# Kernel optimization log

Measured on AMD Instinct MI355X. Metric: run time of the kernel, lower is better.

Reference implementation:

```python
import jax, jax.numpy as jnp
import numpy as np

B, W, LOCAL, GLOBAL = 32, 16, 64, 64
EMB, HIDDEN, OUT, NLAYERS = 256, 512, 64, 3
T = 128  # output_len


def setup_inputs() -> dict:
    key = jax.random.key(0)
    ks = jax.random.split(key, 16)
    s = 0.05
    inp = {
        "z_t": jax.random.normal(ks[0], (B, W, LOCAL), jnp.float32),
        "z_g": jax.random.normal(ks[1], (B, GLOBAL), jnp.float32),
        # embedding: Linear(local+global -> 256, bias=False), torch layout (out,in)
        "w_emb": jax.random.normal(ks[2], (EMB, LOCAL + GLOBAL), jnp.float32) * s,
        # GRU(input_size=1, hidden=256); input is all-zeros so w_ih contributes
        # nothing (only its bias b_ih matters) -> faithfully omit w_ih.
        "gru_w_hh": jax.random.normal(ks[3], (3 * EMB, EMB), jnp.float32) * s,
        "gru_b_ih": jax.random.normal(ks[4], (3 * EMB,), jnp.float32) * s,
        "gru_b_hh": jax.random.normal(ks[5], (3 * EMB,), jnp.float32) * s,
        "mlp_w1": jax.random.normal(ks[6], (HIDDEN, EMB), jnp.float32) * s,
        "mlp_b1": jax.random.normal(ks[7], (HIDDEN,), jnp.float32) * s,
        "mlp_w2": jax.random.normal(ks[8], (HIDDEN, HIDDEN), jnp.float32) * s,
        "mlp_b2": jax.random.normal(ks[9], (HIDDEN,), jnp.float32) * s,
        "mlp_w3": jax.random.normal(ks[10], (HIDDEN, HIDDEN), jnp.float32) * s,
        "mlp_b3": jax.random.normal(ks[11], (HIDDEN,), jnp.float32) * s,
        "mu_w": jax.random.normal(ks[12], (OUT, HIDDEN), jnp.float32) * s,
        "mu_b": jax.random.normal(ks[13], (OUT,), jnp.float32) * s,
        "output_len": T,
    }
    return inp


def _gru_zero_input(h0, w_hh, b_ih, b_hh, length):
    # PyTorch GRU cell with x_t == 0: input-to-hidden term reduces to b_ih.
    b_ir, b_iz, b_in = jnp.split(b_ih, 3)

    def step(h, _):
        gh = h @ w_hh.T + b_hh              # (BW, 3*EMB)
        g_r, g_z, g_n = jnp.split(gh, 3, axis=-1)
        r = jax.nn.sigmoid(b_ir + g_r)
        z = jax.nn.sigmoid(b_iz + g_z)
        n = jnp.tanh(b_in + r * g_n)
        h_new = (1.0 - z) * n + z * h
        return h_new, h_new

    _, hs = jax.lax.scan(step, h0, None, length=length)
    return hs  # (T, BW, EMB)


def reference(z_t, z_g, w_emb, gru_w_hh, gru_b_ih, gru_b_hh,
              mlp_w1, mlp_b1, mlp_w2, mlp_b2, mlp_w3, mlp_b3,
              mu_w, mu_b, output_len):
    b, nw, _ = z_t.shape
    z = jnp.concatenate(
        [z_t, jnp.broadcast_to(z_g[:, None, :], (b, nw, z_g.shape[-1]))], axis=-1)
    emb = z @ w_emb.T                        # (B, W, EMB)
    h0 = emb.reshape(b * nw, -1)             # (BW, EMB) initial hidden state

    hs = _gru_zero_input(h0, gru_w_hh, gru_b_ih, gru_b_hh, output_len)
    h_t = jnp.transpose(hs, (1, 0, 2))       # (BW, T, EMB), batch_first

    # MLP: Linear+ELU (Dropout p=0.05 is identity in eval)
    h = jax.nn.elu(h_t @ mlp_w1.T + mlp_b1)
    h = jax.nn.elu(h @ mlp_w2.T + mlp_b2)
    h = jax.nn.elu(h @ mlp_w3.T + mlp_b3)
    x_mean = h @ mu_w.T + mu_b               # (BW, T, OUT)
    return x_mean.reshape(b, nw * output_len, -1)
```

## Files before the change

kernel.cpp:

```cpp
#include <hip/hip_runtime.h>
#include <hip/hip_bf16.h>


typedef __bf16 bf16_t;
typedef __bf16 bf16x2 __attribute__((ext_vector_type(2)));
typedef __bf16 bf16x8 __attribute__((ext_vector_type(8)));
typedef float f32x4 __attribute__((ext_vector_type(4)));

#define MFMA16(a, b, c) __builtin_amdgcn_mfma_f32_16x16x32_bf16(a, b, c, 0, 0, 0)

#define EMB 256
#define TSTEPS 128
#define OUTD 64

#define HS_OFF   0u
#define H0_OFF   33554432u
#define WHH_OFF  34078720u
#define W1_OFF   34471936u
#define W2_OFF   34734080u
#define W3_OFF   35258368u
#define MUW_OFF  35782656u

__device__ __forceinline__ float rcpf(float x){ return __builtin_amdgcn_rcpf(x); }
__device__ __forceinline__ void lds_barrier() {
  asm volatile("s_waitcnt lgkmcnt(0)\n\ts_barrier" ::: "memory");
}

template<int KC>
__device__ __forceinline__ void conv_frag(
    const float* __restrict__ src, bf16_t* __restrict__ dst,
    int NK, int g, int G)
{
  const int K = KC * 128;
  for (int i = g; i < NK; i += G) {
    const int e    = i & 7;
    const int lane = (i >> 3) & 63;
    const int kk   = (i >> 9) & 3;
    const int rem  = i >> 11;
    const int kc   = rem & (KC - 1);
    const int nt   = rem / KC;
    const int l15  = lane & 15, quad = lane >> 4;
    dst[i] = (bf16_t)src[(size_t)(nt * 16 + l15) * K + kc * 128 + kk * 32 + quad * 8 + e];
  }
}

__global__ __launch_bounds__(256) void convert_kernel(
    const float* __restrict__ whh, const float* __restrict__ w1,
    const float* __restrict__ w2, const float* __restrict__ w3,
    const float* __restrict__ muw, char* __restrict__ ws)
{
  const int g = blockIdx.x * 256 + threadIdx.x;
  const int G = gridDim.x * 256;
  bf16_t* d;
  d = (bf16_t*)(ws + WHH_OFF); for (int i = g; i < 196608; i += G) d[i] = (bf16_t)whh[i];
  conv_frag<2>(w1,  (bf16_t*)(ws + W1_OFF),  131072, g, G);
  conv_frag<4>(w2,  (bf16_t*)(ws + W2_OFF),  262144, g, G);
  conv_frag<4>(w3,  (bf16_t*)(ws + W3_OFF),  262144, g, G);
  conv_frag<4>(muw, (bf16_t*)(ws + MUW_OFF), 32768,  g, G);
}

__global__ __launch_bounds__(256) void emb_kernel(
    const float* __restrict__ z_t, const float* __restrict__ z_g,
    const float* __restrict__ w_emb, float* __restrict__ h0)
{
  __shared__ float zrow[128];
  const int bw = blockIdx.x, tid = threadIdx.x;
  if (tid < 128)
    zrow[tid] = (tid < 64) ? z_t[bw * 64 + tid] : z_g[(bw >> 4) * 64 + (tid - 64)];
  __syncthreads();
  const float4* wp = reinterpret_cast<const float4*>(w_emb + (size_t)tid * 128);
  float s = 0.f;
#pragma unroll
  for (int k4 = 0; k4 < 32; ++k4) {
    const float4 w = wp[k4];
    s += zrow[k4 * 4 + 0] * w.x + zrow[k4 * 4 + 1] * w.y
       + zrow[k4 * 4 + 2] * w.z + zrow[k4 * 4 + 3] * w.w;
  }
  h0[(size_t)bw * 256 + tid] = s;
}

__global__ __launch_bounds__(256, 1) void gru_kernel(
    const float* __restrict__ h0, const bf16_t* __restrict__ w_hh,
    const float* __restrict__ b_ih, const float* __restrict__ b_hh,
    bf16_t* __restrict__ hs)
{
  __shared__ __align__(16) bf16_t h16[2][16][264];

  const int tid  = threadIdx.x;
  const int wv   = tid >> 6;
  const int lane = tid & 63;
  const int l15  = lane & 15;
  const int quad = lane >> 4;
  const int bw0  = blockIdx.x * 4;
  const int c0   = wv * 16 + l15;

  bf16x8 wA[8][8];
#pragma unroll
  for (int ct = 0; ct < 8; ++ct) {
    const int n = (ct >> 2) * 256 + (ct & 3) * 64 + c0;
#pragma unroll
    for (int kk = 0; kk < 8; ++kk)
      wA[ct][kk] = *reinterpret_cast<const bf16x8*>(
          w_hh + (size_t)n * 256 + kk * 32 + quad * 8);
  }
  bf16x8 wV[4][8];
#pragma unroll
  for (int j = 0; j < 4; ++j) {
    const int n = 512 + j * 64 + c0;
#pragma unroll
    for (int kk = 0; kk < 8; ++kk)
      wV[j][kk] = *reinterpret_cast<const bf16x8*>(
          w_hh + (size_t)n * 256 + kk * 32 + quad * 8);
  }

  float br[4], bz[4], bin[4], bhn[4], hm[4];
#pragma unroll
  for (int j = 0; j < 4; ++j) {
    const int c = c0 + j * 64;
    br[j]  = b_ih[c]       + b_hh[c];
    bz[j]  = b_ih[256 + c] + b_hh[256 + c];
    bin[j] = b_ih[512 + c];
    bhn[j] = b_hh[512 + c];
    hm[j]  = h0[(size_t)(bw0 + quad) * 256 + c];
  }

  {
    bf16x8 zv;
#pragma unroll
    for (int e = 0; e < 8; ++e) zv[e] = (bf16_t)0.f;
    for (int i = tid; i < 1056; i += 256)
      reinterpret_cast<bf16x8*>(h16)[i] = zv;
  }
  __syncthreads();
#pragma unroll
  for (int j = 0; j < 4; ++j)
    h16[0][quad * 4][c0 + j * 64] = (bf16_t)hm[j];
  __syncthreads();

  bf16_t* hsp = hs + ((size_t)(bw0 + quad) * TSTEPS) * EMB + c0;

#pragma unroll 1
  for (int t = 0; t < TSTEPS; ++t) {
    const bf16_t (*hr)[264] = h16[t & 1];
    bf16_t (*hw)[264] = h16[(t & 1) ^ 1];

    bf16x8 a8[8];
#pragma unroll
    for (int kk = 0; kk < 8; ++kk)
      a8[kk] = *reinterpret_cast<const bf16x8*>(&hr[l15][kk * 32 + quad * 8]);

    f32x4 acc[12] = {};
    __builtin_amdgcn_sched_barrier(0);
    asm volatile("s_nop 1" :::);

#pragma unroll
    for (int kk = 0; kk < 8; ++kk) {
#pragma unroll
      for (int ct = 0; ct < 8; ++ct)
        asm("v_mfma_f32_16x16x32_bf16 %0, %1, %2, %0"
            : "+v"(acc[ct]) : "v"(a8[kk]), "a"(wA[ct][kk]));
#pragma unroll
      for (int j = 0; j < 4; ++j)
        acc[8 + j] = MFMA16(a8[kk], wV[j][kk], acc[8 + j]);
    }

    __builtin_amdgcn_sched_barrier(0);
    asm volatile("s_nop 7\n\ts_nop 7\n\ts_nop 1" :::);
    __builtin_amdgcn_sched_barrier(0);

#pragma unroll
    for (int j = 0; j < 4; ++j) {
      const float gr = acc[j][0]     + br[j];
      const float gz = acc[4 + j][0] + bz[j];
      const float gn = acc[8 + j][0] + bhn[j];
      const float rr = rcpf(1.f + __expf(-gr));
      const float zz = rcpf(1.f + __expf(-gz));
      const float pre = bin[j] + rr * gn;
      const float nn = 1.f - 2.f * rcpf(__expf(2.f * pre) + 1.f);
      hm[j] = nn + zz * (hm[j] - nn);
      const bf16_t nh = (bf16_t)hm[j];
      hw[quad * 4][c0 + j * 64] = nh;
      hsp[(size_t)t * EMB + j * 64] = nh;
    }
    lds_barrier();
  }
}

template<int KC>
__device__ __forceinline__ void mlp_layer(
    const bf16_t* __restrict__ Wf, const float* __restrict__ bias,
    bf16_t (*act)[520], int wv, int lane, int l15, int quad)
{
  constexpr int NIT = KC * 4;
  f32x4 acc[8][4] = {};
  bf16x8 wf[2][8];

#pragma unroll
  for (int ct = 0; ct < 8; ++ct)
    wf[0][ct] = *reinterpret_cast<const bf16x8*>(
        Wf + (((size_t)(wv * 8 + ct) * KC) << 11) + lane * 8);

#pragma unroll
  for (int it = 0; it < NIT; ++it) {
    const int cur = it & 1, nxt = cur ^ 1;
    if (it + 1 < NIT) {
      const int kc1 = (it + 1) >> 2, kk1 = (it + 1) & 3;
#pragma unroll
      for (int ct = 0; ct < 8; ++ct)
        wf[nxt][ct] = *reinterpret_cast<const bf16x8*>(
            Wf + ((((size_t)(wv * 8 + ct) * KC + kc1) * 4 + kk1) << 9) + lane * 8);
    }
    const int kc = it >> 2, kk = it & 3;
    bf16x8 a8[4];
#pragma unroll
    for (int mt = 0; mt < 4; ++mt)
      a8[mt] = *reinterpret_cast<const bf16x8*>(
          &act[mt * 16 + l15][kc * 128 + kk * 32 + quad * 8]);
#pragma unroll
    for (int mt = 0; mt < 4; ++mt)
#pragma unroll
      for (int ct = 0; ct < 8; ++ct)
        acc[ct][mt] = MFMA16(a8[mt], wf[cur][ct], acc[ct][mt]);
  }

  __syncthreads();
#pragma unroll
  for (int ct = 0; ct < 8; ++ct) {
    const int n = wv * 128 + ct * 16 + l15;
    const float b = bias[n];
#pragma unroll
    for (int mt = 0; mt < 4; ++mt)
#pragma unroll
      for (int r = 0; r < 4; ++r) {
        float x = acc[ct][mt][r] + b;
        x = (x > 0.f) ? x : (__expf(x) - 1.f);
        act[mt * 16 + quad * 4 + r][n] = (bf16_t)x;
      }
  }
  __syncthreads();
}

__global__ __launch_bounds__(256, 2) void mlp_kernel(
    const bf16_t* __restrict__ hs,
    const bf16_t* __restrict__ w1, const float* __restrict__ b1,
    const bf16_t* __restrict__ w2, const float* __restrict__ b2,
    const bf16_t* __restrict__ w3, const float* __restrict__ b3,
    const bf16_t* __restrict__ muw, const float* __restrict__ mub,
    float* __restrict__ out)
{
  __shared__ __align__(16) bf16_t act[64][520];

  const int tid  = threadIdx.x;
  const int wv   = tid >> 6;
  const int lane = tid & 63;
  const int l15  = lane & 15;
  const int quad = lane >> 4;
  const size_t r0 = (size_t)blockIdx.x * 64;

  for (int v = tid; v < 64 * 32; v += 256) {
    const int rr = v >> 5, cc = v & 31;
    bf16x8 x = *reinterpret_cast<const bf16x8*>(hs + (r0 + rr) * EMB + cc * 8);
    *reinterpret_cast<bf16x8*>(&act[rr][cc * 8]) = x;
  }
  __syncthreads();

  mlp_layer<2>(w1, b1, act, wv, lane, l15, quad);
  mlp_layer<4>(w2, b2, act, wv, lane, l15, quad);
  mlp_layer<4>(w3, b3, act, wv, lane, l15, quad);

  f32x4 macc[4] = {};
  const int n = wv * 16 + l15;
#pragma unroll
  for (int it = 0; it < 16; ++it) {
    const int kc = it >> 2, kk = it & 3;
    bf16x8 wfm = *reinterpret_cast<const bf16x8*>(
        muw + ((((size_t)wv * 4 + kc) * 4 + kk) << 9) + lane * 8);
#pragma unroll
    for (int i = 0; i < 4; ++i) {
      bf16x8 a = *reinterpret_cast<const bf16x8*>(
          &act[i * 16 + l15][kc * 128 + kk * 32 + quad * 8]);
      macc[i] = MFMA16(a, wfm, macc[i]);
    }
  }
  const float mb = mub[n];
#pragma unroll
  for (int i = 0; i < 4; ++i)
#pragma unroll
    for (int r = 0; r < 4; ++r)
      out[(r0 + i * 16 + quad * 4 + r) * OUTD + n] = macc[i][r] + mb;
}

extern "C" void kernel_launch(void* const* d_in, const int* in_sizes, int n_in,
                              void* d_out, int out_size, void* d_ws, size_t ws_size,
                              hipStream_t stream) {
  char* ws = (char*)d_ws;

  convert_kernel<<<256, 256, 0, stream>>>(
      (const float*)d_in[3], (const float*)d_in[6], (const float*)d_in[8],
      (const float*)d_in[10], (const float*)d_in[12], ws);

  emb_kernel<<<512, 256, 0, stream>>>(
      (const float*)d_in[0], (const float*)d_in[1], (const float*)d_in[2],
      (float*)(ws + H0_OFF));

  gru_kernel<<<128, 256, 0, stream>>>(
      (const float*)(ws + H0_OFF), (const bf16_t*)(ws + WHH_OFF),
      (const float*)d_in[4], (const float*)d_in[5],
      (bf16_t*)(ws + HS_OFF));

  mlp_kernel<<<1024, 256, 0, stream>>>(
      (const bf16_t*)(ws + HS_OFF),
      (const bf16_t*)(ws + W1_OFF), (const float*)d_in[7],
      (const bf16_t*)(ws + W2_OFF), (const float*)d_in[9],
      (const bf16_t*)(ws + W3_OFF), (const float*)d_in[11],
      (const bf16_t*)(ws + MUW_OFF), (const float*)d_in[13],
      (float*)d_out);
}
```

Measured before the change: 346.3 us.

## Split GRU columns across 8 waves and transpose MLP MFMA for vectorized epilogue

The GRU kernel now runs 512 threads (8 waves) per block, with each wave owning 32 hidden columns and 6 weight fragments instead of 12. This cuts per-step serial MFMA latency and register pressure, and drops the hand-written AGPR asm and s_nop padding. In the MLP, the MFMA operands are swapped so each lane holds 4 consecutive output columns. The bias add, ELU and stores can then use float4/bf16x4 vector accesses instead of scalar scattered writes. The cost is more waves contending on the per-step barrier and LDS reads.

```diff
diff --git a/kernel.cpp b/kernel.cpp
--- a/kernel.cpp
+++ b/kernel.cpp
@@ -4,6 +4,7 @@
 
 typedef __bf16 bf16_t;
 typedef __bf16 bf16x2 __attribute__((ext_vector_type(2)));
+typedef __bf16 bf16x4 __attribute__((ext_vector_type(4)));
 typedef __bf16 bf16x8 __attribute__((ext_vector_type(8)));
 typedef float f32x4 __attribute__((ext_vector_type(4)));
 
@@ -24,6 +25,9 @@
 __device__ __forceinline__ float rcpf(float x){ return __builtin_amdgcn_rcpf(x); }
 __device__ __forceinline__ void lds_barrier() {
   asm volatile("s_waitcnt lgkmcnt(0)\n\ts_barrier" ::: "memory");
+}
+__device__ __forceinline__ float eluf(float x) {
+  return (x > 0.f) ? x : (__expf(x) - 1.f);
 }
 
 template<int KC>
@@ -79,7 +83,7 @@
   h0[(size_t)bw * 256 + tid] = s;
 }
 
-__global__ __launch_bounds__(256, 1) void gru_kernel(
+__global__ __launch_bounds__(512, 2) void gru_kernel(
     const float* __restrict__ h0, const bf16_t* __restrict__ w_hh,
     const float* __restrict__ b_ih, const float* __restrict__ b_hh,
     bf16_t* __restrict__ hs)
@@ -92,95 +96,73 @@
   const int l15  = lane & 15;
   const int quad = lane >> 4;
   const int bw0  = blockIdx.x * 4;
-  const int c0   = wv * 16 + l15;
-
-  bf16x8 wA[8][8];
-#pragma unroll
-  for (int ct = 0; ct < 8; ++ct) {
-    const int n = (ct >> 2) * 256 + (ct & 3) * 64 + c0;
-#pragma unroll
-    for (int kk = 0; kk < 8; ++kk)
-      wA[ct][kk] = *reinterpret_cast<const bf16x8*>(
-          w_hh + (size_t)n * 256 + kk * 32 + quad * 8);
-  }
-  bf16x8 wV[4][8];
-#pragma unroll
-  for (int j = 0; j < 4; ++j) {
-    const int n = 512 + j * 64 + c0;
-#pragma unroll
-    for (int kk = 0; kk < 8; ++kk)
-      wV[j][kk] = *reinterpret_cast<const bf16x8*>(
-          w_hh + (size_t)n * 256 + kk * 32 + quad * 8);
-  }
-
-  float br[4], bz[4], bin[4], bhn[4], hm[4];
-#pragma unroll
-  for (int j = 0; j < 4; ++j) {
-    const int c = c0 + j * 64;
-    br[j]  = b_ih[c]       + b_hh[c];
-    bz[j]  = b_ih[256 + c] + b_hh[256 + c];
-    bin[j] = b_ih[512 + c];
-    bhn[j] = b_hh[512 + c];
-    hm[j]  = h0[(size_t)(bw0 + quad) * 256 + c];
+  const int cA   = wv * 32 + l15;
+
+  bf16x8 wf[6][8];
+#pragma unroll
+  for (int g = 0; g < 3; ++g)
+#pragma unroll
+    for (int s = 0; s < 2; ++s) {
+      const int n = g * 256 + cA + s * 16;
+#pragma unroll
+      for (int kk = 0; kk < 8; ++kk)
+        wf[g * 2 + s][kk] = *reinterpret_cast<const bf16x8*>(
+            w_hh + (size_t)n * 256 + kk * 32 + quad * 8);
+    }
+
+  float br[2], bz[2], bin[2], bhn[2], hm[2];
+#pragma unroll
+  for (int s = 0; s < 2; ++s) {
+    const int c = cA + s * 16;
+    br[s]  = b_ih[c]       + b_hh[c];
+    bz[s]  = b_ih[256 + c] + b_hh[256 + c];
+    bin[s] = b_ih[512 + c];
+    bhn[s] = b_hh[512 + c];
+    hm[s]  = h0[(size_t)(bw0 + quad) * 256 + c];
   }
 
   {
     bf16x8 zv;
 #pragma unroll
     for (int e = 0; e < 8; ++e) zv[e] = (bf16_t)0.f;
-    for (int i = tid; i < 1056; i += 256)
+    for (int i = tid; i < 1056; i += 512)
       reinterpret_cast<bf16x8*>(h16)[i] = zv;
   }
   __syncthreads();
 #pragma unroll
-  for (int j = 0; j < 4; ++j)
-    h16[0][quad * 4][c0 + j * 64] = (bf16_t)hm[j];
-  __syncthreads();
-
-  bf16_t* hsp = hs + ((size_t)(bw0 + quad) * TSTEPS) * EMB + c0;
+  for (int s = 0; s < 2; ++s)
+    h16[0][quad * 4][cA + s * 16] = (bf16_t)hm[s];
+  __syncthreads();
+
+  bf16_t* hsp = hs + ((size_t)(bw0 + quad) * TSTEPS) * EMB + cA;
 
 #pragma unroll 1
   for (int t = 0; t < TSTEPS; ++t) {
     const bf16_t (*hr)[264] = h16[t & 1];
     bf16_t (*hw)[264] = h16[(t & 1) ^ 1];
 
-    bf16x8 a8[8];
-#pragma unroll
-    for (int kk = 0; kk < 8; ++kk)
-      a8[kk] = *reinterpret_cast<const bf16x8*>(&hr[l15][kk * 32 + quad * 8]);
-
-    f32x4 acc[12] = {};
-    __builtin_amdgcn_sched_barrier(0);
-    asm volatile("s_nop 1" :::);
-
+    f32x4 acc[6] = {};
 #pragma unroll
     for (int kk = 0; kk < 8; ++kk) {
-#pragma unroll
-      for (int ct = 0; ct < 8; ++ct)
-        asm("v_mfma_f32_16x16x32_bf16 %0, %1, %2, %0"
-            : "+v"(acc[ct]) : "v"(a8[kk]), "a"(wA[ct][kk]));
-#pragma unroll
-      for (int j = 0; j < 4; ++j)
-        acc[8 + j] = MFMA16(a8[kk], wV[j][kk], acc[8 + j]);
-    }
-
-    __builtin_amdgcn_sched_barrier(0);
-    asm volatile("s_nop 7\n\ts_nop 7\n\ts_nop 1" :::);
-    __builtin_amdgcn_sched_barrier(0);
-
-#pragma unroll
-    for (int j = 0; j < 4; ++j) {
-      const float gr = acc[j][0]     + br[j];
-      const float gz = acc[4 + j][0] + bz[j];
-      const float gn = acc[8 + j][0] + bhn[j];
+      const bf16x8 a = *reinterpret_cast<const bf16x8*>(&hr[l15][kk * 32 + quad * 8]);
+#pragma unroll
+      for (int ct = 0; ct < 6; ++ct)
+        acc[ct] = MFMA16(a, wf[ct][kk], acc[ct]);
+    }
+
+#pragma unroll
+    for (int s = 0; s < 2; ++s) {
+      const float gr = acc[s][0]     + br[s];
+      const float gz = acc[2 + s][0] + bz[s];
+      const float gn = acc[4 + s][0] + bhn[s];
       const float rr = rcpf(1.f + __expf(-gr));
       const float zz = rcpf(1.f + __expf(-gz));
-      const float pre = bin[j] + rr * gn;
+      const float pre = bin[s] + rr * gn;
       const float nn = 1.f - 2.f * rcpf(__expf(2.f * pre) + 1.f);
-      hm[j] = nn + zz * (hm[j] - nn);
-      const bf16_t nh = (bf16_t)hm[j];
-      hw[quad * 4][c0 + j * 64] = nh;
-      hsp[(size_t)t * EMB + j * 64] = nh;
+      hm[s] = nn + zz * (hm[s] - nn);
+      const bf16_t nh = (bf16_t)hm[s];
+      hw[quad * 4][cA + s * 16] = nh;
+      hsp[(size_t)t * EMB + s * 16] = nh;
     }
     lds_barrier();
   }
@@ -220,22 +202,23 @@
     for (int mt = 0; mt < 4; ++mt)
 #pragma unroll
       for (int ct = 0; ct < 8; ++ct)
-        acc[ct][mt] = MFMA16(a8[mt], wf[cur][ct], acc[ct][mt]);
+        acc[ct][mt] = MFMA16(wf[cur][ct], a8[mt], acc[ct][mt]);
   }
 
   __syncthreads();
 #pragma unroll
   for (int ct = 0; ct < 8; ++ct) {
-    const int n = wv * 128 + ct * 16 + l15;
-    const float b = bias[n];
-#pragma unroll
-    for (int mt = 0; mt < 4; ++mt)
-#pragma unroll
-      for (int r = 0; r < 4; ++r) {
-        float x = acc[ct][mt][r] + b;
-        x = (x > 0.f) ? x : (__expf(x) - 1.f);
-        act[mt * 16 + quad * 4 + r][n] = (bf16_t)x;
-      }
+    const int nb = (wv * 8 + ct) * 16 + quad * 4;
+    const float4 b4 = *reinterpret_cast<const float4*>(bias + nb);
+#pragma unroll
+    for (int mt = 0; mt < 4; ++mt) {
+      bf16x4 v;
+      v[0] = (bf16_t)eluf(acc[ct][mt][0] + b4.x);
+      v[1] = (bf16_t)eluf(acc[ct][mt][1] + b4.y);
+      v[2] = (bf16_t)eluf(acc[ct][mt][2] + b4.z);
+      v[3] = (bf16_t)eluf(acc[ct][mt][3] + b4.w);
+      *reinterpret_cast<bf16x4*>(&act[mt * 16 + l15][nb]) = v;
+    }
   }
   __syncthreads();
 }
@@ -269,7 +252,6 @@
   mlp_layer<4>(w3, b3, act, wv, lane, l15, quad);
 
   f32x4 macc[4] = {};
-  const int n = wv * 16 + l15;
 #pragma unroll
   for (int it = 0; it < 16; ++it) {
     const int kc = it >> 2, kk = it & 3;
@@ -279,15 +261,20 @@
     for (int i = 0; i < 4; ++i) {
       bf16x8 a = *reinterpret_cast<const bf16x8*>(
           &act[i * 16 + l15][kc * 128 + kk * 32 + quad * 8]);
-      macc[i] = MFMA16(a, wfm, macc[i]);
-    }
-  }
-  const float mb = mub[n];
-#pragma unroll
-  for (int i = 0; i < 4; ++i)
-#pragma unroll
-    for (int r = 0; r < 4; ++r)
-      out[(r0 + i * 16 + quad * 4 + r) * OUTD + n] = macc[i][r] + mb;
+      macc[i] = MFMA16(wfm, a, macc[i]);
+    }
+  }
+  const int nb = wv * 16 + quad * 4;
+  const float4 mb4 = *reinterpret_cast<const float4*>(mub + nb);
+#pragma unroll
+  for (int i = 0; i < 4; ++i) {
+    float4 o;
+    o.x = macc[i][0] + mb4.x;
+    o.y = macc[i][1] + mb4.y;
+    o.z = macc[i][2] + mb4.z;
+    o.w = macc[i][3] + mb4.w;
+    *reinterpret_cast<float4*>(out + (r0 + i * 16 + l15) * OUTD + nb) = o;
+  }
 }
 
 extern "C" void kernel_launch(void* const* d_in, const int* in_sizes, int n_in,
@@ -303,7 +290,7 @@
       (const float*)d_in[0], (const float*)d_in[1], (const float*)d_in[2],
       (float*)(ws + H0_OFF));
 
-  gru_kernel<<<128, 256, 0, stream>>>(
+  gru_kernel<<<128, 512, 0, stream>>>(
       (const float*)(ws + H0_OFF), (const bf16_t*)(ws + WHH_OFF),
       (const float*)d_in[4], (const float*)d_in[5],
       (bf16_t*)(ws + HS_OFF));
```

Result: faster. 334.3 us (-3.5%).
